# Performance work log

Hardware: AMD Instinct MI355X
Metric: run time of the kernel (lower is better)

The kernel has to match this reference:

```python
import jax, jax.numpy as jnp
import numpy as np

B, S, D_MODEL = 1, 2048, 2048
N_HEADS, N_KV_HEADS, D_HEAD = 16, 4, 128
ROTARY_DIM, ROTARY_BASE = 128, 10000.0
ATTN_SCALE = float(np.sqrt(D_HEAD))
REPEAT = N_HEADS // N_KV_HEADS


def _sin_cos_rotary(n_ctx, rotary_dim, base):
    # TransformerLens calculate_sin_cos_rotary, rotary_adjacent_pairs=False:
    # freq repeated as 'd -> (2 d)'
    pos = jnp.arange(n_ctx, dtype=jnp.float32)
    dim = jnp.arange(rotary_dim // 2, dtype=jnp.float32)
    freq = base ** (dim / (rotary_dim / 2))
    freq = jnp.concatenate([freq, freq])  # (2 d)
    angles = pos[:, None] / freq[None, :]  # [n_ctx, rotary_dim]
    return jnp.sin(angles), jnp.cos(angles)


def _rotate_every_two_half(x):
    # rotate_half for non-adjacent pairs: [-x2, x1]
    d = x.shape[-1]
    return jnp.concatenate([-x[..., d // 2:], x[..., : d // 2]], axis=-1)


def _apply_rotary(x, sin, cos):
    # x: [batch, pos, head, d_head]; sin/cos: [n_ctx, rotary_dim]
    p = x.shape[1]
    s = sin[:p][:, None, :]  # [pos, 1, rotary_dim]
    c = cos[:p][:, None, :]
    x_rot = x[..., :ROTARY_DIM]
    x_pass = x[..., ROTARY_DIM:]
    x_rotated = x_rot * c + _rotate_every_two_half(x_rot) * s
    return jnp.concatenate([x_rotated, x_pass], axis=-1)


def setup_inputs() -> dict:
    key = jax.random.key(0)
    ks = jax.random.split(key, 10)
    init = 1.0 / np.sqrt(D_MODEL)
    return {
        "query_input": jax.random.normal(ks[0], (B, S, D_MODEL), jnp.float32),
        "key_input": jax.random.normal(ks[1], (B, S, D_MODEL), jnp.float32),
        "value_input": jax.random.normal(ks[2], (B, S, D_MODEL), jnp.float32),
        "W_Q": jax.random.normal(ks[3], (N_HEADS, D_MODEL, D_HEAD), jnp.float32) * init,
        "b_Q": jnp.zeros((N_HEADS, D_HEAD), jnp.float32),
        "W_K": jax.random.normal(ks[4], (N_KV_HEADS, D_MODEL, D_HEAD), jnp.float32) * init,
        "b_K": jnp.zeros((N_KV_HEADS, D_HEAD), jnp.float32),
        "W_V": jax.random.normal(ks[5], (N_KV_HEADS, D_MODEL, D_HEAD), jnp.float32) * init,
        "b_V": jnp.zeros((N_KV_HEADS, D_HEAD), jnp.float32),
        "W_O": jax.random.normal(ks[6], (N_HEADS, D_HEAD, D_MODEL), jnp.float32) * init,
        "b_O": jnp.zeros((D_MODEL,), jnp.float32),
    }


def reference(query_input, key_input, value_input, W_Q, b_Q, W_K, b_K, W_V, b_V, W_O, b_O):
    sin, cos = _sin_cos_rotary(S, ROTARY_DIM, ROTARY_BASE)

    # Projections
    q = jnp.einsum("bpd,hdk->bphk", query_input, W_Q) + b_Q   # [B,S,H,dh]
    k = jnp.einsum("bpd,hdk->bphk", key_input, W_K) + b_K     # [B,S,Hkv,dh]
    v = jnp.einsum("bpd,hdk->bphk", value_input, W_V) + b_V   # [B,S,Hkv,dh]

    # Rotary on q and k (before KV head expansion)
    q = _apply_rotary(q, sin, cos)
    k = _apply_rotary(k, sin, cos)

    # GQA expansion via repeat_interleave on head dim
    k = jnp.repeat(k, REPEAT, axis=2)  # [B,S,H,dh]
    v = jnp.repeat(v, REPEAT, axis=2)

    # Attention scores, causal mask, softmax
    scores = jnp.einsum("bqhd,bkhd->bhqk", q, k) / ATTN_SCALE  # [B,H,S,S]
    causal = jnp.tril(jnp.ones((S, S), dtype=bool))
    scores = jnp.where(causal, scores, jnp.finfo(scores.dtype).min)
    pattern = jax.nn.softmax(scores, axis=-1)

    # Weighted values and output projection
    z = jnp.einsum("bhqk,bkhd->bqhd", pattern, v)              # [B,S,H,dh]
    out = jnp.einsum("bqhd,hdm->bqm", z, W_O) + b_O            # [B,S,D]
    return out
```

## Files before the change

### kernel.cpp

```cpp
#include <hip/hip_runtime.h>
#include <hip/hip_bf16.h>
#include <stdint.h>
#include <math.h>

typedef __bf16 bf16_t;
typedef __attribute__((ext_vector_type(8))) __bf16 bf16x8;
typedef __attribute__((ext_vector_type(4))) __bf16 bf16x4;
typedef __attribute__((ext_vector_type(4))) float f32x4;

static constexpr int S = 2048;
static constexpr int DM = 2048;
static constexpr int NH = 16;
static constexpr int NKV = 4;
static constexpr int DH = 128;

#define MFMA16(a, b, c) __builtin_amdgcn_mfma_f32_16x16x32_bf16((a), (b), (c), 0, 0, 0)

__device__ __forceinline__ void gload_lds16(const void* g, void* l) {
  __builtin_amdgcn_global_load_lds((__attribute__((address_space(1))) void*)(g),
                                   (__attribute__((address_space(3))) void*)(l), 16, 0, 0);
}

template <int N>
__device__ __forceinline__ void wait_vmcnt() {
  asm volatile("s_waitcnt vmcnt(%0)" :: "n"(N) : "memory");
}
__device__ __forceinline__ void wait_lgkm0() {
  asm volatile("s_waitcnt lgkmcnt(0)" ::: "memory");
}

__global__ void rope_table_k(float2* __restrict__ tab) {
  int p = blockIdx.x;
  int j = threadIdx.x;
  double inv = exp2(-(double)j * 13.287712379549449 / 64.0);
  double ang = (double)p * inv;
  tab[p * 64 + j] = make_float2((float)sin(ang), (float)cos(ang));
}

__global__ void cvt3_k(const float* __restrict__ Xq, const float* __restrict__ Xk,
                       const float* __restrict__ Xv, bf16_t* __restrict__ xq,
                       bf16_t* __restrict__ xk, bf16_t* __restrict__ xv) {
  int i = (blockIdx.x * 256 + threadIdx.x) * 4;
  const float* in; bf16_t* out; int off;
  if (i < 4194304) { in = Xq; out = xq; off = i; }
  else if (i < 8388608) { in = Xk; out = xk; off = i - 4194304; }
  else { in = Xv; out = xv; off = i - 8388608; }
  f32x4 v = *(const f32x4*)(in + off);
  bf16x4 o;
  o[0] = (bf16_t)v[0]; o[1] = (bf16_t)v[1]; o[2] = (bf16_t)v[2]; o[3] = (bf16_t)v[3];
  *(bf16x4*)(out + off) = o;
}

__global__ void transpose_w_k(const float* __restrict__ in, bf16_t* __restrict__ out,
                              int R, int C, int rb, int cb, int ldo) {
  __shared__ float tile[32][33];
  int b = blockIdx.z;
  int c0 = blockIdx.x * 32, r0 = blockIdx.y * 32;
  int tx = threadIdx.x, ty = threadIdx.y;
  const float* src = in + (size_t)b * R * C;
  #pragma unroll
  for (int j = 0; j < 32; j += 8)
    tile[ty + j][tx] = src[(size_t)(r0 + ty + j) * C + c0 + tx];
  __syncthreads();
  #pragma unroll
  for (int j = 0; j < 32; j += 8) {
    int c = c0 + ty + j;
    int r = r0 + tx;
    out[(size_t)(b * rb + c) * ldo + b * cb + r] = (bf16_t)tile[tx][ty + j];
  }
}

__global__ void transpose_wkv_k(const float* __restrict__ WK, const float* __restrict__ WV,
                                bf16_t* __restrict__ wkT, bf16_t* __restrict__ wvT) {
  __shared__ float tile[32][33];
  int z = blockIdx.z;
  int b = z & 3;
  const float* in = (z < 4) ? WK : WV;
  bf16_t* out = (z < 4) ? wkT : wvT;
  int c0 = blockIdx.x * 32, r0 = blockIdx.y * 32;
  int tx = threadIdx.x, ty = threadIdx.y;
  const float* src = in + (size_t)b * 2048 * 128;
  #pragma unroll
  for (int j = 0; j < 32; j += 8)
    tile[ty + j][tx] = src[(size_t)(r0 + ty + j) * 128 + c0 + tx];
  __syncthreads();
  #pragma unroll
  for (int j = 0; j < 32; j += 8) {
    int c = c0 + ty + j;
    int r = r0 + tx;
    out[(size_t)(b * 128 + c) * 2048 + r] = (bf16_t)tile[tx][ty + j];
  }
}

__global__ void transpose_v_k(const bf16_t* __restrict__ in, bf16_t* __restrict__ out,
                              int R, int C) {
  __shared__ bf16_t tile[32][33];
  int b = blockIdx.z;
  int c0 = blockIdx.x * 32, r0 = blockIdx.y * 32;
  int tx = threadIdx.x, ty = threadIdx.y;
  const bf16_t* src = in + (size_t)b * R * C;
  bf16_t* dst = out + (size_t)b * R * C;
  #pragma unroll
  for (int j = 0; j < 32; j += 8)
    tile[ty + j][tx] = src[(size_t)(r0 + ty + j) * C + c0 + tx];
  __syncthreads();
  #pragma unroll
  for (int j = 0; j < 32; j += 8)
    dst[(size_t)(c0 + ty + j) * R + r0 + tx] = tile[tx][ty + j];
}

__global__ void rope_qk_k(bf16_t* __restrict__ Qb, bf16_t* __restrict__ Kb,
                          const float2* __restrict__ tab, float qscale) {
  int tid = blockIdx.x * 256 + threadIdx.x;
  int row = tid >> 4;
  int i = (tid & 15) * 4;
  bf16_t* base; float scale;
  if (row < NH * S) { base = Qb + (size_t)row * DH; scale = qscale; }
  else { base = Kb + (size_t)(row - NH * S) * DH; scale = 1.0f; }
  int p = row & (S - 1);
  bf16x4 lo = *(bf16x4*)(base + i);
  bf16x4 hi = *(bf16x4*)(base + i + 64);
  float4 t0 = *(const float4*)(tab + p * 64 + i);
  float4 t1 = *(const float4*)(tab + p * 64 + i + 2);
  float sv[4] = {t0.x, t0.z, t1.x, t1.z};
  float cv[4] = {t0.y, t0.w, t1.y, t1.w};
  bf16x4 nlo, nhi;
  #pragma unroll
  for (int j = 0; j < 4; ++j) {
    float a = (float)lo[j], b = (float)hi[j];
    nlo[j] = (bf16_t)((a * cv[j] - b * sv[j]) * scale);
    nhi[j] = (bf16_t)((b * cv[j] + a * sv[j]) * scale);
  }
  *(bf16x4*)(base + i) = nlo;
  *(bf16x4*)(base + i + 64) = nhi;
}

__global__ __launch_bounds__(256)
void proj_gemm_k(const bf16_t* __restrict__ xq, const bf16_t* __restrict__ xk,
                 const bf16_t* __restrict__ xv, const bf16_t* __restrict__ wqT,
                 const bf16_t* __restrict__ wkT, const bf16_t* __restrict__ wvT,
                 const float* __restrict__ bQ, const float* __restrict__ bK,
                 const float* __restrict__ bV, bf16_t* __restrict__ Qb,
                 bf16_t* __restrict__ Kb, bf16_t* __restrict__ Vb) {
  const int nb = blockIdx.x;
  const int m0 = blockIdx.y * 128;
  const bf16_t* A; const bf16_t* B; const float* bias; bf16_t* dst; int ncol0;
  if (nb < 32)      { A = xq; B = wqT; bias = bQ; dst = Qb; ncol0 = nb * 64; }
  else if (nb < 40) { A = xk; B = wkT; bias = bK; dst = Kb; ncol0 = (nb - 32) * 64; }
  else              { A = xv; B = wvT; bias = bV; dst = Vb; ncol0 = (nb - 40) * 64; }
  const int K = 2048;
  const int t = threadIdx.x;
  const int lane = t & 63, w = t >> 6;
  const int l15 = lane & 15, lg = lane >> 4;
  const int wr = (w >> 1) * 64, wc = (w & 1) * 32;

  __shared__ bf16_t lA[2][128 * 64];
  __shared__ bf16_t lB[2][64 * 64];

  f32x4 acc[4][2] = {};
  const int srow = t >> 3;
  const int sslot = t & 7;

  auto stage = [&](int buf, int kt) {
    #pragma unroll
    for (int i = 0; i < 4; ++i) {
      int row = i * 32 + srow;
      int ss = sslot ^ (row & 7);
      gload_lds16(A + (size_t)(m0 + row) * K + kt * 64 + ss * 8,
                  (void*)(&lA[buf][0] + i * 2048 + t * 8));
    }
    #pragma unroll
    for (int i = 0; i < 2; ++i) {
      int row = i * 32 + srow;
      int ss = sslot ^ (row & 7);
      gload_lds16(B + (size_t)(ncol0 + row) * K + kt * 64 + ss * 8,
                  (void*)(&lB[buf][0] + i * 2048 + t * 8));
    }
  };

  const int nk = K >> 6;
  stage(0, 0);
  for (int kt = 0; kt < nk; ++kt) {
    const int cur = kt & 1;
    if (kt + 1 < nk) {
      stage(cur ^ 1, kt + 1);
      wait_vmcnt<6>();
    } else {
      wait_vmcnt<0>();
    }
    __builtin_amdgcn_s_barrier();
    #pragma unroll
    for (int kk = 0; kk < 2; ++kk) {
      bf16x8 af[4], bfv[2];
      #pragma unroll
      for (int f = 0; f < 4; ++f) {
        int row = wr + f * 16 + l15;
        int slot = kk * 4 + lg;
        af[f] = *(const bf16x8*)(&lA[cur][0] + row * 64 + ((slot ^ (row & 7)) * 8));
      }
      #pragma unroll
      for (int f = 0; f < 2; ++f) {
        int row = wc + f * 16 + l15;
        int slot = kk * 4 + lg;
        bfv[f] = *(const bf16x8*)(&lB[cur][0] + row * 64 + ((slot ^ (row & 7)) * 8));
      }
      #pragma unroll
      for (int fm = 0; fm < 4; ++fm)
        #pragma unroll
        for (int fn = 0; fn < 2; ++fn)
          acc[fm][fn] = MFMA16(af[fm], bfv[fn], acc[fm][fn]);
    }
    wait_lgkm0();
    __builtin_amdgcn_s_barrier();
  }

  #pragma unroll
  for (int fm = 0; fm < 4; ++fm) {
    int rowb = m0 + wr + fm * 16 + lg * 4;
    #pragma unroll
    for (int fn = 0; fn < 2; ++fn) {
      int col = ncol0 + wc + fn * 16 + l15;
      float bb = bias[col];
      #pragma unroll
      for (int r = 0; r < 4; ++r) {
        float v = acc[fm][fn][r] + bb;
        int rr = rowb + r;
        dst[((size_t)(col >> 7) * S + rr) * DH + (col & 127)] = (bf16_t)v;
      }
    }
  }
}

__global__ __launch_bounds__(256)
void gemm_o_k(const bf16_t* __restrict__ A, const bf16_t* __restrict__ B,
              const float* __restrict__ bias, float* __restrict__ Cout) {
  const int ncol0 = blockIdx.x * 64;
  const int m0 = blockIdx.y * 128;
  const int K = 2048;
  const int t = threadIdx.x;
  const int lane = t & 63, w = t >> 6;
  const int l15 = lane & 15, lg = lane >> 4;
  const int wr = (w >> 1) * 64, wc = (w & 1) * 32;

  __shared__ bf16_t lA[2][128 * 64];
  __shared__ bf16_t lB[2][64 * 64];

  f32x4 acc[4][2] = {};
  const int srow = t >> 3;
  const int sslot = t & 7;

  auto stage = [&](int buf, int kt) {
    #pragma unroll
    for (int i = 0; i < 4; ++i) {
      int row = i * 32 + srow;
      int ss = sslot ^ (row & 7);
      gload_lds16(A + (size_t)(m0 + row) * K + kt * 64 + ss * 8,
                  (void*)(&lA[buf][0] + i * 2048 + t * 8));
    }
    #pragma unroll
    for (int i = 0; i < 2; ++i) {
      int row = i * 32 + srow;
      int ss = sslot ^ (row & 7);
      gload_lds16(B + (size_t)(ncol0 + row) * K + kt * 64 + ss * 8,
                  (void*)(&lB[buf][0] + i * 2048 + t * 8));
    }
  };

  const int nk = K >> 6;
  stage(0, 0);
  for (int kt = 0; kt < nk; ++kt) {
    const int cur = kt & 1;
    if (kt + 1 < nk) {
      stage(cur ^ 1, kt + 1);
      wait_vmcnt<6>();
    } else {
      wait_vmcnt<0>();
    }
    __builtin_amdgcn_s_barrier();
    #pragma unroll
    for (int kk = 0; kk < 2; ++kk) {
      bf16x8 af[4], bfv[2];
      #pragma unroll
      for (int f = 0; f < 4; ++f) {
        int row = wr + f * 16 + l15;
        int slot = kk * 4 + lg;
        af[f] = *(const bf16x8*)(&lA[cur][0] + row * 64 + ((slot ^ (row & 7)) * 8));
      }
      #pragma unroll
      for (int f = 0; f < 2; ++f) {
        int row = wc + f * 16 + l15;
        int slot = kk * 4 + lg;
        bfv[f] = *(const bf16x8*)(&lB[cur][0] + row * 64 + ((slot ^ (row & 7)) * 8));
      }
      #pragma unroll
      for (int fm = 0; fm < 4; ++fm)
        #pragma unroll
        for (int fn = 0; fn < 2; ++fn)
          acc[fm][fn] = MFMA16(af[fm], bfv[fn], acc[fm][fn]);
    }
    wait_lgkm0();
    __builtin_amdgcn_s_barrier();
  }

  #pragma unroll
  for (int fm = 0; fm < 4; ++fm) {
    int rowb = m0 + wr + fm * 16 + lg * 4;
    #pragma unroll
    for (int fn = 0; fn < 2; ++fn) {
      int col = ncol0 + wc + fn * 16 + l15;
      float bb = bias[col];
      #pragma unroll
      for (int r = 0; r < 4; ++r)
        Cout[(size_t)(rowb + r) * DM + col] = acc[fm][fn][r] + bb;
    }
  }
}

__global__ __launch_bounds__(256)
void attn_k(const bf16_t* __restrict__ Q, const bf16_t* __restrict__ K,
            const bf16_t* __restrict__ Vt, bf16_t* __restrict__ Z) {
  const int lin = blockIdx.x;
  const int h = lin & 15;
  const int ip = lin >> 4;
  const int qblk = (ip < 16) ? ip : 47 - ip;
  const int q0 = qblk * 64;
  const int hkv = h >> 2;
  const int t = threadIdx.x;
  const int lane = t & 63, w = t >> 6;
  const int l15 = lane & 15, lg = lane >> 4;

  __shared__ bf16_t lK[2][64 * 128];
  __shared__ bf16_t lV[2][128 * 64];
  __shared__ bf16_t lP[4][16 * 64];

  const int qrow = q0 + w * 16 + l15;
  bf16x8 qf[4];
  #pragma unroll
  for (int kk = 0; kk < 4; ++kk)
    qf[kk] = *(const bf16x8*)(Q + ((size_t)h * S + qrow) * DH + kk * 32 + lg * 8);

  auto stageKV = [&](int buf, int kt) {
    #pragma unroll
    for (int i = 0; i < 4; ++i) {
      int row = i * 16 + (t >> 4);
      int ss = (t & 15) ^ (row & 15);
      gload_lds16(K + ((size_t)hkv * S + kt * 64 + row) * DH + ss * 8,
                  (void*)(&lK[buf][0] + i * 2048 + t * 8));
    }
    #pragma unroll
    for (int i = 0; i < 4; ++i) {
      int row = i * 32 + (t >> 3);
      int ss = (t & 7) ^ (row & 7);
      gload_lds16(Vt + ((size_t)hkv * DH + row) * S + kt * 64 + ss * 8,
                  (void*)(&lV[buf][0] + i * 2048 + t * 8));
    }
  };

  f32x4 oacc[8] = {};
  float m_run = -1e30f, l_run = 0.f;

  const int ktmax = q0 >> 6;
  stageKV(0, 0);
  for (int kt = 0; kt <= ktmax; ++kt) {
    const int cur = kt & 1;
    if (kt < ktmax) {
      stageKV(cur ^ 1, kt + 1);
      wait_vmcnt<8>();
    } else {
      wait_vmcnt<0>();
    }
    __builtin_amdgcn_s_barrier();

    f32x4 sacc[4] = {};
    __builtin_amdgcn_s_setprio(1);
    #pragma unroll
    for (int kk = 0; kk < 4; ++kk) {
      #pragma unroll
      for (int fm = 0; fm < 4; ++fm) {
        int row = fm * 16 + l15;
        int slot = kk * 4 + lg;
        bf16x8 kf = *(const bf16x8*)(&lK[cur][0] + row * 128 + ((slot ^ (row & 15)) * 8));
        sacc[fm] = MFMA16(kf, qf[kk], sacc[fm]);
      }
    }
    __builtin_amdgcn_s_setprio(0);

    const bool diag = (kt == ktmax);
    float smax = -1e30f;
    #pragma unroll
    for (int fm = 0; fm < 4; ++fm) {
      #pragma unroll
      for (int r = 0; r < 4; ++r) {
        float s = sacc[fm][r];
        if (diag) {
          int keyg = kt * 64 + fm * 16 + lg * 4 + r;
          if (keyg > qrow) s = -1e30f;
        }
        sacc[fm][r] = s;
        smax = fmaxf(smax, s);
      }
    }
    smax = fmaxf(smax, __shfl_xor(smax, 16));
    smax = fmaxf(smax, __shfl_xor(smax, 32));

    float m_new, alpha;
    bool noresc = __all(smax - m_run <= 8.0f);
    if (noresc) {
      m_new = m_run;
      alpha = 1.0f;
    } else {
      m_new = fmaxf(m_run, smax);
      alpha = exp2f(m_run - m_new);
    }

    float psum = 0.f;
    #pragma unroll
    for (int fm = 0; fm < 4; ++fm) {
      bf16x4 pk;
      #pragma unroll
      for (int r = 0; r < 4; ++r) {
        float p = exp2f(sacc[fm][r] - m_new);
        psum += p;
        pk[r] = (bf16_t)p;
      }
      int slot = fm * 2 + (lg >> 1);
      char* dst = (char*)(&lP[w][0]) + l15 * 128 + ((slot ^ (l15 & 7)) * 16) + ((lg & 1) * 8);
      *(bf16x4*)dst = pk;
    }
    psum += __shfl_xor(psum, 16);
    psum += __shfl_xor(psum, 32);
    l_run = l_run * alpha + psum;
    m_run = m_new;

    if (!noresc) {
      #pragma unroll
      for (int r = 0; r < 4; ++r) {
        float ar = __shfl(alpha, lg * 4 + r);
        #pragma unroll
        for (int n = 0; n < 8; ++n) oacc[n][r] *= ar;
      }
    }

    __builtin_amdgcn_s_setprio(1);
    #pragma unroll
    for (int kk2 = 0; kk2 < 2; ++kk2) {
      int pslot = kk2 * 4 + lg;
      bf16x8 pf = *(const bf16x8*)((char*)(&lP[w][0]) + l15 * 128 + ((pslot ^ (l15 & 7)) * 16));
      #pragma unroll
      for (int n = 0; n < 8; ++n) {
        int vrow = n * 16 + l15;
        int vslot = kk2 * 4 + lg;
        bf16x8 vf = *(const bf16x8*)(&lV[cur][0] + vrow * 64 + ((vslot ^ (vrow & 7)) * 8));
        oacc[n] = MFMA16(pf, vf, oacc[n]);
      }
    }
    __builtin_amdgcn_s_setprio(0);
    wait_lgkm0();
    __builtin_amdgcn_s_barrier();
  }

  #pragma unroll
  for (int r = 0; r < 4; ++r) {
    float lr = __shfl(l_run, lg * 4 + r);
    float inv = 1.0f / lr;
    int qg = q0 + w * 16 + lg * 4 + r;
    #pragma unroll
    for (int n = 0; n < 8; ++n) {
      int d = n * 16 + l15;
      Z[(size_t)qg * DM + h * DH + d] = (bf16_t)(oacc[n][r] * inv);
    }
  }
}

extern "C" void kernel_launch(void* const* d_in, const int* in_sizes, int n_in,
                              void* d_out, int out_size, void* d_ws, size_t ws_size,
                              hipStream_t stream) {
  (void)in_sizes; (void)n_in; (void)out_size; (void)ws_size;
  const float* Xq = (const float*)d_in[0];
  const float* Xk = (const float*)d_in[1];
  const float* Xv = (const float*)d_in[2];
  const float* WQ = (const float*)d_in[3];
  const float* bQ = (const float*)d_in[4];
  const float* WK = (const float*)d_in[5];
  const float* bK = (const float*)d_in[6];
  const float* WV = (const float*)d_in[7];
  const float* bV = (const float*)d_in[8];
  const float* WO = (const float*)d_in[9];
  const float* bO = (const float*)d_in[10];

  char* w = (char*)d_ws;
  float2* tab = (float2*)w;
  bf16_t* xq  = (bf16_t*)(w + (1 << 20));
  bf16_t* xk  = xq + 4194304;
  bf16_t* xv  = xk + 4194304;
  bf16_t* wqT = xv + 4194304;
  bf16_t* wkT = wqT + 4194304;
  bf16_t* wvT = wkT + 1048576;
  bf16_t* woT = wvT + 1048576;
  bf16_t* Qb  = woT + 4194304;
  bf16_t* Kb  = Qb + 4194304;
  bf16_t* Vb  = Kb + 1048576;
  bf16_t* Vtb = Vb + 1048576;
  bf16_t* Zb  = Vtb + 1048576;

  rope_table_k<<<dim3(S), dim3(64), 0, stream>>>(tab);
  cvt3_k<<<dim3(12288), dim3(256), 0, stream>>>(Xq, Xk, Xv, xq, xk, xv);
  transpose_w_k<<<dim3(4, 64, 16), dim3(32, 8), 0, stream>>>(WQ, wqT, 2048, 128, 128, 0, 2048);
  transpose_wkv_k<<<dim3(4, 64, 8), dim3(32, 8), 0, stream>>>(WK, WV, wkT, wvT);
  transpose_w_k<<<dim3(64, 4, 16), dim3(32, 8), 0, stream>>>(WO, woT, 128, 2048, 0, 128, 2048);

  proj_gemm_k<<<dim3(48, 16), dim3(256), 0, stream>>>(xq, xk, xv, wqT, wkT, wvT,
                                                      bQ, bK, bV, Qb, Kb, Vb);

  transpose_v_k<<<dim3(4, 64, 4), dim3(32, 8), 0, stream>>>(Vb, Vtb, 2048, 128);

  const float qscale = 1.4426950408889634f / sqrtf(128.0f);
  rope_qk_k<<<dim3(2560), dim3(256), 0, stream>>>(Qb, Kb, tab, qscale);

  attn_k<<<dim3(512), dim3(256), 0, stream>>>(Qb, Kb, Vtb, Zb);

  gemm_o_k<<<dim3(32, 16), dim3(256), 0, stream>>>(Zb, woT, bO, (float*)d_out);
}
```

Measured before the change: 170.2 us.

## Split long causal attention rows across two KV chunks and write V transposed directly

Query blocks 16-31 now have their KV range split into two chunks processed by separate workgroups. A new combine kernel merges the partial outputs using the saved row max and sum. This balances causal work across more blocks (768 instead of 512) to cut tail imbalance. Separately, the projection GEMM now writes V already transposed with packed stores, which removes the separate transpose kernel. The costs are the fp32 partial-output traffic and one extra launch. The partials reuse the bf16 input-conversion buffer as scratch.

After: 159.3 us. -6.4%, faster.

```diff
diff --git a/kernel.cpp b/kernel.cpp
--- a/kernel.cpp
+++ b/kernel.cpp
@@ -90,23 +90,6 @@
     int r = r0 + tx;
     out[(size_t)(b * 128 + c) * 2048 + r] = (bf16_t)tile[tx][ty + j];
   }
-}
-
-__global__ void transpose_v_k(const bf16_t* __restrict__ in, bf16_t* __restrict__ out,
-                              int R, int C) {
-  __shared__ bf16_t tile[32][33];
-  int b = blockIdx.z;
-  int c0 = blockIdx.x * 32, r0 = blockIdx.y * 32;
-  int tx = threadIdx.x, ty = threadIdx.y;
-  const bf16_t* src = in + (size_t)b * R * C;
-  bf16_t* dst = out + (size_t)b * R * C;
-  #pragma unroll
-  for (int j = 0; j < 32; j += 8)
-    tile[ty + j][tx] = src[(size_t)(r0 + ty + j) * C + c0 + tx];
-  __syncthreads();
-  #pragma unroll
-  for (int j = 0; j < 32; j += 8)
-    dst[(size_t)(c0 + ty + j) * R + r0 + tx] = tile[tx][ty + j];
 }
 
 __global__ void rope_qk_k(bf16_t* __restrict__ Qb, bf16_t* __restrict__ Kb,
@@ -141,13 +124,14 @@
                  const bf16_t* __restrict__ wkT, const bf16_t* __restrict__ wvT,
                  const float* __restrict__ bQ, const float* __restrict__ bK,
                  const float* __restrict__ bV, bf16_t* __restrict__ Qb,
-                 bf16_t* __restrict__ Kb, bf16_t* __restrict__ Vb) {
+                 bf16_t* __restrict__ Kb, bf16_t* __restrict__ Vt) {
   const int nb = blockIdx.x;
   const int m0 = blockIdx.y * 128;
   const bf16_t* A; const bf16_t* B; const float* bias; bf16_t* dst; int ncol0;
+  bool vmode = false;
   if (nb < 32)      { A = xq; B = wqT; bias = bQ; dst = Qb; ncol0 = nb * 64; }
   else if (nb < 40) { A = xk; B = wkT; bias = bK; dst = Kb; ncol0 = (nb - 32) * 64; }
-  else              { A = xv; B = wvT; bias = bV; dst = Vb; ncol0 = (nb - 40) * 64; }
+  else              { A = xv; B = wvT; bias = bV; dst = Vt; ncol0 = (nb - 40) * 64; vmode = true; }
   const int K = 2048;
   const int t = threadIdx.x;
   const int lane = t & 63, w = t >> 6;
@@ -221,11 +205,17 @@
     for (int fn = 0; fn < 2; ++fn) {
       int col = ncol0 + wc + fn * 16 + l15;
       float bb = bias[col];
-      #pragma unroll
-      for (int r = 0; r < 4; ++r) {
-        float v = acc[fm][fn][r] + bb;
-        int rr = rowb + r;
-        dst[((size_t)(col >> 7) * S + rr) * DH + (col & 127)] = (bf16_t)v;
+      if (vmode) {
+        bf16x4 pk;
+        #pragma unroll
+        for (int r = 0; r < 4; ++r) pk[r] = (bf16_t)(acc[fm][fn][r] + bb);
+        *(bf16x4*)(dst + (size_t)col * S + rowb) = pk;
+      } else {
+        #pragma unroll
+        for (int r = 0; r < 4; ++r) {
+          float v = acc[fm][fn][r] + bb;
+          dst[((size_t)(col >> 7) * S + (rowb + r)) * DH + (col & 127)] = (bf16_t)v;
+        }
       }
     }
   }
@@ -318,12 +308,21 @@
 
 __global__ __launch_bounds__(256)
 void attn_k(const bf16_t* __restrict__ Q, const bf16_t* __restrict__ K,
-            const bf16_t* __restrict__ Vt, bf16_t* __restrict__ Z) {
-  const int lin = blockIdx.x;
-  const int h = lin & 15;
-  const int ip = lin >> 4;
-  const int qblk = (ip < 16) ? ip : 47 - ip;
-  const int q0 = qblk * 64;
+            const bf16_t* __restrict__ Vt, bf16_t* __restrict__ Z,
+            float* __restrict__ Opart, float* __restrict__ mpart,
+            float* __restrict__ lpart) {
+  const int bid = blockIdx.x;
+  const int h = bid & 15;
+  const int g = bid >> 4;
+  int qb, ch;
+  if (g <= 16) { qb = 31 - g; ch = 0; }
+  else if (g == 17) { qb = 31; ch = 1; }
+  else {
+    int idx = (g - 18) >> 1;
+    if (g & 1) { ch = 1; qb = 30 - idx; }
+    else { ch = 0; qb = 14 - idx; }
+  }
+  const int q0 = qb * 64;
   const int hkv = h >> 2;
   const int t = threadIdx.x;
   const int lane = t & 63, w = t >> 6;
@@ -359,11 +358,12 @@
   f32x4 oacc[8] = {};
   float m_run = -1e30f, l_run = 0.f;
 
-  const int ktmax = q0 >> 6;
-  stageKV(0, 0);
-  for (int kt = 0; kt <= ktmax; ++kt) {
-    const int cur = kt & 1;
-    if (kt < ktmax) {
+  const int kt0 = ch * 16;
+  const int ktend = ch ? qb : ((qb < 15) ? qb : 15);
+  stageKV(0, kt0);
+  for (int kt = kt0; kt <= ktend; ++kt) {
+    const int cur = (kt - kt0) & 1;
+    if (kt < ktend) {
       stageKV(cur ^ 1, kt + 1);
       wait_vmcnt<8>();
     } else {
@@ -385,7 +385,7 @@
     }
     __builtin_amdgcn_s_setprio(0);
 
-    const bool diag = (kt == ktmax);
+    const bool diag = (kt == qb);
     float smax = -1e30f;
     #pragma unroll
     for (int fm = 0; fm < 4; ++fm) {
@@ -459,17 +459,52 @@
     __builtin_amdgcn_s_barrier();
   }
 
-  #pragma unroll
-  for (int r = 0; r < 4; ++r) {
-    float lr = __shfl(l_run, lg * 4 + r);
-    float inv = 1.0f / lr;
-    int qg = q0 + w * 16 + lg * 4 + r;
-    #pragma unroll
-    for (int n = 0; n < 8; ++n) {
-      int d = n * 16 + l15;
-      Z[(size_t)qg * DM + h * DH + d] = (bf16_t)(oacc[n][r] * inv);
-    }
-  }
+  if (qb < 16) {
+    #pragma unroll
+    for (int r = 0; r < 4; ++r) {
+      float lr = __shfl(l_run, lg * 4 + r);
+      float inv = 1.0f / lr;
+      int qg = q0 + w * 16 + lg * 4 + r;
+      #pragma unroll
+      for (int n = 0; n < 8; ++n) {
+        int d = n * 16 + l15;
+        Z[(size_t)qg * DM + h * DH + d] = (bf16_t)(oacc[n][r] * inv);
+      }
+    }
+  } else {
+    const int slot = (h * 16 + (qb - 16)) * 2 + ch;
+    float* Op = Opart + (size_t)slot * 8192;
+    #pragma unroll
+    for (int r = 0; r < 4; ++r) {
+      int lr = w * 16 + lg * 4 + r;
+      #pragma unroll
+      for (int n = 0; n < 8; ++n)
+        Op[lr * 128 + n * 16 + l15] = oacc[n][r];
+    }
+    if (lg == 0) {
+      mpart[slot * 64 + w * 16 + l15] = m_run;
+      lpart[slot * 64 + w * 16 + l15] = l_run;
+    }
+  }
+}
+
+__global__ void combine_k(const float* __restrict__ Opart, const float* __restrict__ mpart,
+                          const float* __restrict__ lpart, bf16_t* __restrict__ Z) {
+  int idx = blockIdx.x * 256 + threadIdx.x;
+  int d = idx & 127;
+  int r = (idx >> 7) & 63;
+  int qb16 = (idx >> 13) & 15;
+  int h = idx >> 17;
+  int s0 = (h * 16 + qb16) * 2;
+  float m0 = mpart[s0 * 64 + r], m1 = mpart[(s0 + 1) * 64 + r];
+  float l0 = lpart[s0 * 64 + r], l1 = lpart[(s0 + 1) * 64 + r];
+  float M = fmaxf(m0, m1);
+  float a0 = exp2f(m0 - M), a1 = exp2f(m1 - M);
+  float L = a0 * l0 + a1 * l1;
+  float o0 = Opart[(size_t)s0 * 8192 + r * 128 + d];
+  float o1 = Opart[(size_t)(s0 + 1) * 8192 + r * 128 + d];
+  int qrow = (16 + qb16) * 64 + r;
+  Z[(size_t)qrow * DM + h * DH + d] = (bf16_t)((a0 * o0 + a1 * o1) / L);
 }
 
 extern "C" void kernel_launch(void* const* d_in, const int* in_sizes, int n_in,
@@ -499,9 +534,11 @@
   bf16_t* woT = wvT + 1048576;
   bf16_t* Qb  = woT + 4194304;
   bf16_t* Kb  = Qb + 4194304;
-  bf16_t* Vb  = Kb + 1048576;
-  bf16_t* Vtb = Vb + 1048576;
+  bf16_t* Vtb = Kb + 1048576;
   bf16_t* Zb  = Vtb + 1048576;
+  float* Opart = (float*)xq;
+  float* mpart = Opart + 512 * 8192;
+  float* lpart = mpart + 512 * 64;
 
   rope_table_k<<<dim3(S), dim3(64), 0, stream>>>(tab);
   cvt3_k<<<dim3(12288), dim3(256), 0, stream>>>(Xq, Xk, Xv, xq, xk, xv);
@@ -510,14 +547,13 @@
   transpose_w_k<<<dim3(64, 4, 16), dim3(32, 8), 0, stream>>>(WO, woT, 128, 2048, 0, 128, 2048);
 
   proj_gemm_k<<<dim3(48, 16), dim3(256), 0, stream>>>(xq, xk, xv, wqT, wkT, wvT,
-                                                      bQ, bK, bV, Qb, Kb, Vb);
-
-  transpose_v_k<<<dim3(4, 64, 4), dim3(32, 8), 0, stream>>>(Vb, Vtb, 2048, 128);
+                                                      bQ, bK, bV, Qb, Kb, Vtb);
 
   const float qscale = 1.4426950408889634f / sqrtf(128.0f);
   rope_qk_k<<<dim3(2560), dim3(256), 0, stream>>>(Qb, Kb, tab, qscale);
 
-  attn_k<<<dim3(512), dim3(256), 0, stream>>>(Qb, Kb, Vtb, Zb);
+  attn_k<<<dim3(768), dim3(256), 0, stream>>>(Qb, Kb, Vtb, Zb, Opart, mpart, lpart);
+  combine_k<<<dim3(8192), dim3(256), 0, stream>>>(Opart, mpart, lpart, Zb);
 
   gemm_o_k<<<dim3(32, 16), dim3(256), 0, stream>>>(Zb, woT, bO, (float*)d_out);
 }
```
